# Performance work log

Measured on AMD Instinct MI355X. Metric: run time of the kernel, lower is better.

The kernel has to match this reference:

```python
import jax, jax.numpy as jnp
import numpy as np

B, L, D, N = 2, 2048, 1024, 16
DT_MIN, DT_MAX = 1e-3, 1e-1


def setup_inputs() -> dict:
    key = jax.random.key(0)
    ks = jax.random.split(key, 8)
    u = jax.random.normal(ks[0], (B, L, D), dtype=jnp.float32)
    # torch.nn.Linear weights are (out_features, in_features)
    W_dt = jax.random.normal(ks[1], (D, D), dtype=jnp.float32) * 0.02
    b_dt = jnp.zeros((D,), dtype=jnp.float32)
    W_B = jax.random.normal(ks[2], (D * N, D), dtype=jnp.float32) * 0.02
    b_B = jnp.zeros((D * N,), dtype=jnp.float32)
    W_C = jax.random.normal(ks[3], (D * N, D), dtype=jnp.float32) * 0.02
    b_C = jnp.zeros((D * N,), dtype=jnp.float32)
    # log_A init: log(1..N) broadcast over channels (HiPPO-ish diagonal)
    log_A = jnp.broadcast_to(jnp.log(jnp.arange(1, N + 1, dtype=jnp.float32)), (D, N))
    D_skip = jnp.ones((D,), dtype=jnp.float32)
    lo, hi = float(np.log(DT_MIN)), float(np.log(DT_MAX))
    dt_bias = jax.random.uniform(ks[4], (D,), dtype=jnp.float32) * (hi - lo) + lo
    return {"u": u, "log_A": log_A, "D_skip": D_skip, "dt_bias": dt_bias,
            "W_dt": W_dt, "b_dt": b_dt, "W_B": W_B, "b_B": b_B,
            "W_C": W_C, "b_C": b_C}


def reference(u, log_A, D_skip, dt_bias, W_dt, b_dt, W_B, b_B, W_C, b_C):
    b, l, d = u.shape
    n = log_A.shape[1]
    A = -jnp.exp(log_A)                                   # (d, n), A < 0
    # token-dependent parameters, computed for all timesteps at once
    dt = jax.nn.softplus(u @ W_dt.T + b_dt + dt_bias)     # (b, l, d)
    Bt = (u @ W_B.T + b_B).reshape(b, l, d, n)            # (b, l, d, n)
    Ct = (u @ W_C.T + b_C).reshape(b, l, d, n)            # (b, l, d, n)
    # exact ZOH discretisation
    A_bar = jnp.exp(dt[..., None] * A)                    # (b, l, d, n)
    B_bar = (A_bar - 1.0) / A * Bt                        # (b, l, d, n)
    x_in = B_bar * u[..., None]                           # (b, l, d, n)
    # recurrent scan over time
    def step(h, inp):
        a_t, x_t, c_t = inp                               # each (b, d, n)
        h = a_t * h + x_t
        y_t = jnp.sum(c_t * h, axis=-1)                   # (b, d)
        return h, y_t
    h0 = jnp.zeros((b, d, n), dtype=u.dtype)
    xs = (jnp.moveaxis(A_bar, 1, 0), jnp.moveaxis(x_in, 1, 0), jnp.moveaxis(Ct, 1, 0))
    _, ys = jax.lax.scan(step, h0, xs)                    # ys: (l, b, d)
    y = jnp.moveaxis(ys, 0, 1) + D_skip * u               # (b, l, d)
    return y
```

## Files before the change

### kernel.cpp

```cpp
#include <hip/hip_runtime.h>
#include <hip/hip_bf16.h>
#include <stdint.h>

constexpr int Bb = 2;
constexpr int Ll = 2048;
constexpr int Dd = 1024;
constexpr int Nn = 16;
constexpr int NB = Dd * Nn;
constexpr int SL = 64;
constexpr int NCH = Bb * Dd;
constexpr int KCAT = 3 * Dd;

typedef __bf16 bf16_t;
typedef __bf16 bf16x8 __attribute__((ext_vector_type(8)));
typedef __bf16 bf16x4 __attribute__((ext_vector_type(4)));
typedef float f32x4 __attribute__((ext_vector_type(4)));

__device__ inline void gld_lds16(const void* g, void* l) {
    __builtin_amdgcn_global_load_lds(
        (const __attribute__((address_space(1))) unsigned int*)g,
        (__attribute__((address_space(3))) unsigned int*)l, 16, 0, 0);
}

__global__ __launch_bounds__(256) void cvt_bf16(const float* __restrict__ s,
                                                bf16_t* __restrict__ d, int n4) {
    int i = blockIdx.x * 256 + threadIdx.x;
    const int stride = gridDim.x * 256;
    const float4* s4 = (const float4*)s;
    bf16x4* d4 = (bf16x4*)d;
    for (; i < n4; i += stride) {
        float4 v = s4[i];
        bf16x4 o = {(bf16_t)v.x, (bf16_t)v.y, (bf16_t)v.z, (bf16_t)v.w};
        d4[i] = o;
    }
}

__global__ __launch_bounds__(256) void build_ucat(const float* __restrict__ u,
                                                  bf16_t* __restrict__ ucat) {
    const int i = blockIdx.x * 256 + threadIdx.x;
    const int row = i >> 8;
    const int c = (i & 255) << 2;
    float4 v = ((const float4*)u)[i];
    bf16x4 hi = {(bf16_t)v.x, (bf16_t)v.y, (bf16_t)v.z, (bf16_t)v.w};
    bf16x4 lo = {(bf16_t)(v.x - (float)hi.x), (bf16_t)(v.y - (float)hi.y),
                 (bf16_t)(v.z - (float)hi.z), (bf16_t)(v.w - (float)hi.w)};
    bf16_t* r = ucat + (size_t)row * KCAT;
    *(bf16x4*)(r + c) = hi;
    *(bf16x4*)(r + Dd + c) = lo;
    *(bf16x4*)(r + 2 * Dd + c) = hi;
}

__global__ __launch_bounds__(256) void build_wcat(const float* __restrict__ w,
                                                  bf16_t* __restrict__ wcat) {
    const int i = blockIdx.x * 256 + threadIdx.x;
    const int row = i >> 8;
    const int c = (i & 255) << 2;
    float4 v = ((const float4*)w)[i];
    bf16x4 hi = {(bf16_t)v.x, (bf16_t)v.y, (bf16_t)v.z, (bf16_t)v.w};
    bf16x4 lo = {(bf16_t)(v.x - (float)hi.x), (bf16_t)(v.y - (float)hi.y),
                 (bf16_t)(v.z - (float)hi.z), (bf16_t)(v.w - (float)hi.w)};
    bf16_t* r = wcat + (size_t)row * KCAT;
    *(bf16x4*)(r + c) = hi;
    *(bf16x4*)(r + Dd + c) = hi;
    *(bf16x4*)(r + 2 * Dd + c) = lo;
}

template <int EP, typename OutT>
__global__ __launch_bounds__(256) void gemm_mfma(
    const bf16_t* __restrict__ Abase, int CL, int l0, int K,
    const bf16_t* __restrict__ W, const float* __restrict__ b1,
    const float* __restrict__ b2, OutT* __restrict__ C, int N)
{
    __shared__ bf16_t As[128 * 32];
    __shared__ bf16_t Bs[128 * 32];

    const int tid = threadIdx.x;
    const int bn = blockIdx.x * 128;
    const int rglob = blockIdx.y * 128;
    const int batch = rglob / CL;
    const int rin = rglob % CL;
    const bf16_t* Ap = Abase + ((size_t)batch * Ll + l0 + rin) * K;
    const bf16_t* Wp = W + (size_t)bn * K;
    OutT* Cp = C + (size_t)rglob * N;

    const int sr = tid >> 2;
    const int sc = (tid & 3) << 3;
    char* ldsA = (char*)As + tid * 16;
    char* ldsB = (char*)Bs + tid * 16;

    const int lane = tid & 63;
    const int wid = tid >> 6;
    const int wm = (wid & 1) << 6;
    const int wn = (wid >> 1) << 6;
    const int lr = lane & 15;
    const int lq = lane >> 4;

    f32x4 acc[4][4] = {};

    for (int k0 = 0; k0 < K; k0 += 32) {
        __syncthreads();
        gld_lds16(Ap + (size_t)sr * K + k0 + sc, ldsA);
        gld_lds16(Ap + (size_t)(sr + 64) * K + k0 + sc, ldsA + 4096);
        gld_lds16(Wp + (size_t)sr * K + k0 + sc, ldsB);
        gld_lds16(Wp + (size_t)(sr + 64) * K + k0 + sc, ldsB + 4096);
        __syncthreads();

        bf16x8 af[4], bfr[4];
#pragma unroll
        for (int mi = 0; mi < 4; ++mi)
            af[mi] = *(const bf16x8*)&As[(wm + mi * 16 + lr) * 32 + lq * 8];
#pragma unroll
        for (int ni = 0; ni < 4; ++ni)
            bfr[ni] = *(const bf16x8*)&Bs[(wn + ni * 16 + lr) * 32 + lq * 8];
#pragma unroll
        for (int mi = 0; mi < 4; ++mi)
#pragma unroll
            for (int ni = 0; ni < 4; ++ni)
                acc[mi][ni] = __builtin_amdgcn_mfma_f32_16x16x32_bf16(
                    af[mi], bfr[ni], acc[mi][ni], 0, 0, 0);
    }

#pragma unroll
    for (int ni = 0; ni < 4; ++ni) {
        const int col = bn + wn + ni * 16 + lr;
        const float bc = b1[col] + (EP == 1 ? b2[col] : 0.f);
#pragma unroll
        for (int mi = 0; mi < 4; ++mi)
#pragma unroll
            for (int i = 0; i < 4; ++i) {
                float v = acc[mi][ni][i] + bc;
                if (EP == 1) v = (v > 20.f) ? v : log1pf(__expf(v));
                Cp[(size_t)(wm + mi * 16 + lq * 4 + i) * N + col] = (OutT)v;
            }
    }
}

__global__ __launch_bounds__(512, 2) void gemm256(
    const bf16_t* __restrict__ Abase, int CL, int l0, int K,
    const bf16_t* __restrict__ W, const float* __restrict__ b1,
    bf16_t* __restrict__ C, int N)
{
    extern __shared__ char smem[];
    const int tid = threadIdx.x;
    const int bn = blockIdx.x * 256;
    const int rglob = blockIdx.y * 256;
    const int batch = rglob / CL;
    const int rin = rglob % CL;
    const bf16_t* Ap = Abase + ((size_t)batch * Ll + l0 + rin) * K;
    const bf16_t* Wp = W + (size_t)bn * K;
    bf16_t* Cp = C + (size_t)rglob * N;

    const int lane = tid & 63;
    const int wid = tid >> 6;
    const int wr = wid >> 2;
    const int wc = wid & 3;
    const int lr = lane & 15;
    const int lq = lane >> 4;
    const int NT = K >> 6;

    const int c0 = tid, c1 = tid + 512;
    const int r0 = c0 >> 3, r1 = c1 >> 3;
    const int kb0 = ((c0 & 7) << 3) ^ ((r0 & 7) << 3);
    const int kb1 = ((c1 & 7) << 3) ^ ((r1 & 7) << 3);

    auto stage = [&](const bf16_t* src, char* dst, int tt, int h) {
        gld_lds16(src + (size_t)(h * 128 + r0) * K + tt * 64 + kb0,
                  dst + h * 16384 + c0 * 16);
        gld_lds16(src + (size_t)(h * 128 + r1) * K + tt * 64 + kb1,
                  dst + h * 16384 + c1 * 16);
    };

    stage(Ap, smem, 0, 0);
    stage(Ap, smem, 0, 1);
    stage(Wp, smem + 32768, 0, 0);
    stage(Wp, smem + 32768, 0, 1);
    if (NT > 1) {
        stage(Wp, smem + 65536 + 32768, 1, 0);
        stage(Wp, smem + 65536 + 32768, 1, 1);
        asm volatile("s_waitcnt vmcnt(4)" ::: "memory");
    } else {
        asm volatile("s_waitcnt vmcnt(0)" ::: "memory");
    }
    __builtin_amdgcn_s_barrier();

    f32x4 acc[8][4] = {};
    const int xsw = (lr & 7) << 4;

    for (int t = 0; t < NT; ++t) {
        char* Ard = smem + ((t & 1) ? 65536 : 0);
        char* Brd = Ard + 32768;
        char* Awr = smem + ((t & 1) ? 0 : 65536);
        char* Bwr = Brd;

        bf16x8 bfr[2][4];
#pragma unroll
        for (int p = 0; p < 4; ++p) {
            if (p == 0) { if (t + 1 < NT) stage(Ap, Awr, t + 1, 0); }
            if (p == 1) { if (t + 1 < NT) stage(Ap, Awr, t + 1, 1); }
            if (p == 2) { if (t + 2 < NT) stage(Wp, Bwr, t + 2, 0); }
            if (p == 3) { if (t + 2 < NT) stage(Wp, Bwr, t + 2, 1); }

            if (p == 0) {
#pragma unroll
                for (int ks = 0; ks < 2; ++ks)
#pragma unroll
                    for (int ni = 0; ni < 4; ++ni)
                        bfr[ks][ni] = *(const bf16x8*)(Brd +
                            (wc * 64 + ni * 16 + lr) * 128 +
                            ((ks * 64 + lq * 16) ^ xsw));
            }
            bf16x8 a0k0 = *(const bf16x8*)(Ard +
                (wr * 128 + (2 * p) * 16 + lr) * 128 + ((lq * 16) ^ xsw));
            bf16x8 a0k1 = *(const bf16x8*)(Ard +
                (wr * 128 + (2 * p) * 16 + lr) * 128 + ((64 + lq * 16) ^ xsw));
            bf16x8 a1k0 = *(const bf16x8*)(Ard +
                (wr * 128 + (2 * p + 1) * 16 + lr) * 128 + ((lq * 16) ^ xsw));
            bf16x8 a1k1 = *(const bf16x8*)(Ard +
                (wr * 128 + (2 * p + 1) * 16 + lr) * 128 + ((64 + lq * 16) ^ xsw));

            __builtin_amdgcn_s_barrier();
            __builtin_amdgcn_s_setprio(1);
#pragma unroll
            for (int ni = 0; ni < 4; ++ni) {
                acc[2 * p][ni] = __builtin_amdgcn_mfma_f32_16x16x32_bf16(
                    a0k0, bfr[0][ni], acc[2 * p][ni], 0, 0, 0);
                acc[2 * p][ni] = __builtin_amdgcn_mfma_f32_16x16x32_bf16(
                    a0k1, bfr[1][ni], acc[2 * p][ni], 0, 0, 0);
                acc[2 * p + 1][ni] = __builtin_amdgcn_mfma_f32_16x16x32_bf16(
                    a1k0, bfr[0][ni], acc[2 * p + 1][ni], 0, 0, 0);
                acc[2 * p + 1][ni] = __builtin_amdgcn_mfma_f32_16x16x32_bf16(
                    a1k1, bfr[1][ni], acc[2 * p + 1][ni], 0, 0, 0);
            }
            __builtin_amdgcn_s_setprio(0);
            if (p == 3) {
                if (t + 2 < NT)
                    asm volatile("s_waitcnt vmcnt(4)" ::: "memory");
                else if (t + 1 < NT)
                    asm volatile("s_waitcnt vmcnt(0)" ::: "memory");
            }
            __builtin_amdgcn_s_barrier();
        }
    }

#pragma unroll
    for (int ni = 0; ni < 4; ++ni) {
        const int col = bn + wc * 64 + ni * 16 + lr;
        const float bc = b1[col];
#pragma unroll
        for (int mi = 0; mi < 8; ++mi)
#pragma unroll
            for (int i = 0; i < 4; ++i)
                Cp[(size_t)(wr * 128 + mi * 16 + lq * 4 + i) * N + col] =
                    (bf16_t)(acc[mi][ni][i] + bc);
    }
}

__global__ __launch_bounds__(256) void scan_seg_local(
    const float* __restrict__ u, const float* __restrict__ dt,
    const bf16_t* __restrict__ Bt_c, const float* __restrict__ log_A,
    float* __restrict__ pseg, float* __restrict__ hseg, int CL, int l0)
{
    const int tid = threadIdx.x;
    const int g = tid >> 4, n = tid & 15;
    const int gid = blockIdx.x * 16 + g;
    const int ch = gid & (NCH - 1);
    const int s = gid >> 11;
    const int b = ch >> 10, d = ch & (Dd - 1);

    const float A = -__expf(log_A[d * Nn + n]);
    const float rA = 1.f / A;

    size_t idx_bn = (size_t)(b * CL + s * SL) * NB + d * Nn + n;
    size_t idx_u = ((size_t)b * Ll + l0 + s * SL) * Dd + d;

    float p = 1.f, h = 0.f;
    for (int l = 0; l < SL; ++l) {
        const float dtv = dt[idx_u];
        const float uv = u[idx_u];
        const float bv = (float)Bt_c[idx_bn];
        const float a = __expf(dtv * A);
        p *= a;
        h = a * h + (a - 1.f) * rA * bv * uv;
        idx_bn += NB; idx_u += Dd;
    }
    const size_t o = ((size_t)s * NCH + ch) * Nn + n;
    pseg[o] = p;
    hseg[o] = h;
}

__global__ __launch_bounds__(256) void scan_combine(
    const float* __restrict__ pseg, const float* __restrict__ hseg,
    float* __restrict__ hin_arr, float* __restrict__ h_state,
    int NSEG, int l0)
{
    const int t = blockIdx.x * 256 + threadIdx.x;
    float hin = (l0 == 0) ? 0.f : h_state[t];
    for (int s = 0; s < NSEG; ++s) {
        const size_t o = (size_t)s * (NCH * Nn) + t;
        hin_arr[o] = hin;
        hin = pseg[o] * hin + hseg[o];
    }
    h_state[t] = hin;
}

__global__ __launch_bounds__(256) void scan_seg_final(
    const float* __restrict__ u, const float* __restrict__ dt,
    const bf16_t* __restrict__ Bt_c, const bf16_t* __restrict__ Ct_c,
    const float* __restrict__ log_A, const float* __restrict__ D_skip,
    const float* __restrict__ hin_arr, float* __restrict__ y, int CL, int l0)
{
    const int tid = threadIdx.x;
    const int g = tid >> 4, n = tid & 15;
    const int gid = blockIdx.x * 16 + g;
    const int ch = gid & (NCH - 1);
    const int s = gid >> 11;
    const int b = ch >> 10, d = ch & (Dd - 1);

    const float A = -__expf(log_A[d * Nn + n]);
    const float rA = 1.f / A;
    const float Dsk = D_skip[d];

    size_t idx_bn = (size_t)(b * CL + s * SL) * NB + d * Nn + n;
    size_t idx_u = ((size_t)b * Ll + l0 + s * SL) * Dd + d;

    float h = hin_arr[((size_t)s * NCH + ch) * Nn + n];
    for (int l = 0; l < SL; ++l) {
        const float dtv = dt[idx_u];
        const float uv = u[idx_u];
        const float bv = (float)Bt_c[idx_bn];
        const float cv = (float)Ct_c[idx_bn];
        const float a = __expf(dtv * A);
        h = a * h + (a - 1.f) * rA * bv * uv;
        float p = cv * h;
        p += __shfl_xor(p, 1);
        p += __shfl_xor(p, 2);
        p += __shfl_xor(p, 4);
        p += __shfl_xor(p, 8);
        if (n == 0) y[idx_u] = p + Dsk * uv;
        idx_bn += NB; idx_u += Dd;
    }
}

static inline size_t al256(size_t x) { return (x + 255) & ~(size_t)255; }

extern "C" void kernel_launch(void* const* d_in, const int* in_sizes, int n_in,
                              void* d_out, int out_size, void* d_ws, size_t ws_size,
                              hipStream_t stream) {
    const float* u       = (const float*)d_in[0];
    const float* log_A   = (const float*)d_in[1];
    const float* D_skip  = (const float*)d_in[2];
    const float* dt_bias = (const float*)d_in[3];
    const float* W_dt    = (const float*)d_in[4];
    const float* b_dt    = (const float*)d_in[5];
    const float* W_B     = (const float*)d_in[6];
    const float* b_B     = (const float*)d_in[7];
    const float* W_C     = (const float*)d_in[8];
    const float* b_C     = (const float*)d_in[9];
    float* y = (float*)d_out;

    hipFuncSetAttribute(reinterpret_cast<const void*>(gemm256),
                        hipFuncAttributeMaxDynamicSharedMemorySize, 131072);

    const size_t sz_ubf  = al256((size_t)Bb * Ll * Dd * 2);
    const size_t sz_w    = al256((size_t)NB * Dd * 2);
    const size_t sz_h    = al256((size_t)NCH * Nn * 4);
    const size_t sz_dtf  = al256((size_t)Bb * Ll * Dd * 4);
    const size_t sz_ucat = al256((size_t)Bb * Ll * KCAT * 2);
    const size_t sz_wcat = al256((size_t)Dd * KCAT * 2);

    int CL = 128;
    const int cands[5] = {2048, 1024, 512, 256, 128};
    for (int i = 0; i < 5; ++i) {
        const int c = cands[i];
        const int nseg = c / SL;
        const size_t seg = 3 * al256((size_t)nseg * NCH * Nn * 4);
        const size_t chunk = 2 * al256((size_t)2 * c * NB * 2);
        const size_t ovl = sz_ucat + sz_wcat;
        const size_t need = sz_ubf + 2 * sz_w + sz_h + sz_dtf + seg +
                            (chunk > ovl ? chunk : ovl);
        if (need <= ws_size) { CL = c; break; }
    }
    const int NSEG = CL / SL;

    char* p = (char*)d_ws;
    bf16_t* u_bf   = (bf16_t*)p; p += sz_ubf;
    bf16_t* wB_bf  = (bf16_t*)p; p += sz_w;
    bf16_t* wC_bf  = (bf16_t*)p; p += sz_w;
    float* h_state = (float*)p; p += sz_h;
    float* dt_full = (float*)p; p += sz_dtf;
    const size_t sz_seg1 = al256((size_t)NSEG * NCH * Nn * 4);
    float* pseg    = (float*)p; p += sz_seg1;
    float* hseg    = (float*)p; p += sz_seg1;
    float* hin_arr = (float*)p; p += sz_seg1;
    char* chunk0 = p;
    bf16_t* Bt_c = (bf16_t*)chunk0;
    bf16_t* Ct_c = (bf16_t*)(chunk0 + al256((size_t)2 * CL * NB * 2));
    bf16_t* u_cat = (bf16_t*)chunk0;
    bf16_t* w_cat = (bf16_t*)(chunk0 + sz_ucat);

    cvt_bf16<<<2048, 256, 0, stream>>>(u, u_bf, Bb * Ll * Dd / 4);
    cvt_bf16<<<2048, 256, 0, stream>>>(W_B, wB_bf, NB * Dd / 4);
    cvt_bf16<<<2048, 256, 0, stream>>>(W_C, wC_bf, NB * Dd / 4);
    build_ucat<<<Bb * Ll * Dd / 4 / 256, 256, 0, stream>>>(u, u_cat);
    build_wcat<<<Dd * Dd / 4 / 256, 256, 0, stream>>>(W_dt, w_cat);

    gemm_mfma<1, float><<<dim3(Dd / 128, Bb * Ll / 128), 256, 0, stream>>>(
        u_cat, Ll, 0, KCAT, w_cat, b_dt, dt_bias, dt_full, Dd);

    const bool use256 = (CL % 256 == 0);
    for (int l0 = 0; l0 < Ll; l0 += CL) {
        if (use256) {
            gemm256<<<dim3(NB / 256, 2 * CL / 256), 512, 131072, stream>>>(
                u_bf, CL, l0, Dd, wB_bf, b_B, Bt_c, NB);
            gemm256<<<dim3(NB / 256, 2 * CL / 256), 512, 131072, stream>>>(
                u_bf, CL, l0, Dd, wC_bf, b_C, Ct_c, NB);
        } else {
            gemm_mfma<0, bf16_t><<<dim3(NB / 128, 2 * CL / 128), 256, 0, stream>>>(
                u_bf, CL, l0, Dd, wB_bf, b_B, nullptr, Bt_c, NB);
            gemm_mfma<0, bf16_t><<<dim3(NB / 128, 2 * CL / 128), 256, 0, stream>>>(
                u_bf, CL, l0, Dd, wC_bf, b_C, nullptr, Ct_c, NB);
        }
        scan_seg_local<<<dim3(128 * NSEG), 256, 0, stream>>>(
            u, dt_full, Bt_c, log_A, pseg, hseg, CL, l0);
        scan_combine<<<dim3(128), 256, 0, stream>>>(
            pseg, hseg, hin_arr, h_state, NSEG, l0);
        scan_seg_final<<<dim3(128 * NSEG), 256, 0, stream>>>(
            u, dt_full, Bt_c, Ct_c, log_A, D_skip, hin_arr, y, CL, l0);
    }
}
```

Baseline: 730.5 us.

## Merge B and C projection GEMMs into one launch with swizzled tile order

Replaces the two per-chunk gemm256 launches for the B and C projections with a single gemm256_bc kernel. Each block picks the B or C weight from its flattened block id, using a grouped tile ordering meant to improve L2 reuse of the shared u tiles. The MFMA operands are swapped so each lane holds four consecutive output columns, which lets the epilogue write vectorized bf16x4 stores with float4 bias loads. A separate smaller-tile gemm_dt kernel computes dt with vectorized float4 softplus stores. The cost is more kernel code and a dt kernel with single-buffered LDS staging.

```diff
diff --git a/kernel.cpp b/kernel.cpp
--- a/kernel.cpp
+++ b/kernel.cpp
@@ -135,20 +135,103 @@
     }
 }
 
-__global__ __launch_bounds__(512, 2) void gemm256(
+__global__ __launch_bounds__(256) void gemm_dt(
+    const bf16_t* __restrict__ A, int K, const bf16_t* __restrict__ W,
+    const float* __restrict__ b1, const float* __restrict__ b2,
+    float* __restrict__ C)
+{
+    __shared__ bf16_t As[128 * 32];
+    __shared__ bf16_t Bs[64 * 32];
+
+    const int tid = threadIdx.x;
+    const int bn = blockIdx.x * 64;
+    const int row0 = blockIdx.y * 128;
+    const bf16_t* Ap = A + (size_t)row0 * K;
+    const bf16_t* Wp = W + (size_t)bn * K;
+    float* Cp = C + (size_t)row0 * Dd;
+
+    const int sr = tid >> 2;
+    const int sc = (tid & 3) << 3;
+    char* ldsA = (char*)As + tid * 16;
+    char* ldsB = (char*)Bs + tid * 16;
+
+    const int lane = tid & 63;
+    const int wid = tid >> 6;
+    const int wm = (wid & 1) << 6;
+    const int wn = (wid >> 1) << 5;
+    const int lr = lane & 15;
+    const int lq = lane >> 4;
+
+    f32x4 acc[4][2] = {};
+
+    for (int k0 = 0; k0 < K; k0 += 32) {
+        __syncthreads();
+        gld_lds16(Ap + (size_t)sr * K + k0 + sc, ldsA);
+        gld_lds16(Ap + (size_t)(sr + 64) * K + k0 + sc, ldsA + 4096);
+        gld_lds16(Wp + (size_t)sr * K + k0 + sc, ldsB);
+        __syncthreads();
+
+        bf16x8 af[4], bfr[2];
+#pragma unroll
+        for (int mi = 0; mi < 4; ++mi)
+            af[mi] = *(const bf16x8*)&As[(wm + mi * 16 + lr) * 32 + lq * 8];
+#pragma unroll
+        for (int ni = 0; ni < 2; ++ni)
+            bfr[ni] = *(const bf16x8*)&Bs[(wn + ni * 16 + lr) * 32 + lq * 8];
+#pragma unroll
+        for (int mi = 0; mi < 4; ++mi)
+#pragma unroll
+            for (int ni = 0; ni < 2; ++ni)
+                acc[mi][ni] = __builtin_amdgcn_mfma_f32_16x16x32_bf16(
+                    bfr[ni], af[mi], acc[mi][ni], 0, 0, 0);
+    }
+
+#pragma unroll
+    for (int ni = 0; ni < 2; ++ni) {
+        const int col = bn + wn + ni * 16 + lq * 4;
+        const float4 ba = *(const float4*)&b1[col];
+        const float4 bb = *(const float4*)&b2[col];
+        const float bc[4] = {ba.x + bb.x, ba.y + bb.y, ba.z + bb.z, ba.w + bb.w};
+#pragma unroll
+        for (int mi = 0; mi < 4; ++mi) {
+            const int row = wm + mi * 16 + lr;
+            f32x4 v;
+#pragma unroll
+            for (int i = 0; i < 4; ++i) {
+                float t = acc[mi][ni][i] + bc[i];
+                v[i] = (t > 20.f) ? t : log1pf(__expf(t));
+            }
+            *(f32x4*)(Cp + (size_t)row * Dd + col) = v;
+        }
+    }
+}
+
+__global__ __launch_bounds__(512, 2) void gemm256_bc(
     const bf16_t* __restrict__ Abase, int CL, int l0, int K,
-    const bf16_t* __restrict__ W, const float* __restrict__ b1,
-    bf16_t* __restrict__ C, int N)
+    const bf16_t* __restrict__ WB, const bf16_t* __restrict__ WC,
+    const float* __restrict__ bB, const float* __restrict__ bC,
+    bf16_t* __restrict__ OB, bf16_t* __restrict__ OC)
 {
     extern __shared__ char smem[];
     const int tid = threadIdx.x;
-    const int bn = blockIdx.x * 256;
-    const int rglob = blockIdx.y * 256;
+
+    const int NY = (2 * CL) >> 8;
+    const int id = blockIdx.x;
+    const int cx = id & 7;
+    const int jj = id >> 3;
+    const int x = cx * 16 + jj / NY;
+    const int yb = jj % NY;
+
+    const int rglob = yb * 256;
     const int batch = rglob / CL;
     const int rin = rglob % CL;
     const bf16_t* Ap = Abase + ((size_t)batch * Ll + l0 + rin) * K;
-    const bf16_t* Wp = W + (size_t)bn * K;
-    bf16_t* Cp = C + (size_t)rglob * N;
+
+    const bf16_t* Wp; const float* bias; bf16_t* Co; int bn;
+    if (x < 64) { Wp = WB; bias = bB; Co = OB; bn = x * 256; }
+    else        { Wp = WC; bias = bC; Co = OC; bn = (x - 64) * 256; }
+    Wp += (size_t)bn * K;
+    bf16_t* Cp = Co + (size_t)rglob * NB;
 
     const int lane = tid & 63;
     const int wid = tid >> 6;
@@ -223,13 +306,13 @@
 #pragma unroll
             for (int ni = 0; ni < 4; ++ni) {
                 acc[2 * p][ni] = __builtin_amdgcn_mfma_f32_16x16x32_bf16(
-                    a0k0, bfr[0][ni], acc[2 * p][ni], 0, 0, 0);
+                    bfr[0][ni], a0k0, acc[2 * p][ni], 0, 0, 0);
                 acc[2 * p][ni] = __builtin_amdgcn_mfma_f32_16x16x32_bf16(
-                    a0k1, bfr[1][ni], acc[2 * p][ni], 0, 0, 0);
+                    bfr[1][ni], a0k1, acc[2 * p][ni], 0, 0, 0);
                 acc[2 * p + 1][ni] = __builtin_amdgcn_mfma_f32_16x16x32_bf16(
-                    a1k0, bfr[0][ni], acc[2 * p + 1][ni], 0, 0, 0);
+                    bfr[0][ni], a1k0, acc[2 * p + 1][ni], 0, 0, 0);
                 acc[2 * p + 1][ni] = __builtin_amdgcn_mfma_f32_16x16x32_bf16(
-                    a1k1, bfr[1][ni], acc[2 * p + 1][ni], 0, 0, 0);
+                    bfr[1][ni], a1k1, acc[2 * p + 1][ni], 0, 0, 0);
             }
             __builtin_amdgcn_s_setprio(0);
             if (p == 3) {
@@ -242,16 +325,22 @@
         }
     }
 
-#pragma unroll
-    for (int ni = 0; ni < 4; ++ni) {
-        const int col = bn + wc * 64 + ni * 16 + lr;
-        const float bc = b1[col];
-#pragma unroll
-        for (int mi = 0; mi < 8; ++mi)
-#pragma unroll
-            for (int i = 0; i < 4; ++i)
-                Cp[(size_t)(wr * 128 + mi * 16 + lq * 4 + i) * N + col] =
-                    (bf16_t)(acc[mi][ni][i] + bc);
+    float4 bv[4];
+#pragma unroll
+    for (int ni = 0; ni < 4; ++ni)
+        bv[ni] = *(const float4*)&bias[bn + wc * 64 + ni * 16 + lq * 4];
+#pragma unroll
+    for (int mi = 0; mi < 8; ++mi) {
+        const size_t rowoff = (size_t)(wr * 128 + mi * 16 + lr) * NB;
+#pragma unroll
+        for (int ni = 0; ni < 4; ++ni) {
+            const int col = bn + wc * 64 + ni * 16 + lq * 4;
+            bf16x4 o = {(bf16_t)(acc[mi][ni][0] + bv[ni].x),
+                        (bf16_t)(acc[mi][ni][1] + bv[ni].y),
+                        (bf16_t)(acc[mi][ni][2] + bv[ni].z),
+                        (bf16_t)(acc[mi][ni][3] + bv[ni].w)};
+            *(bf16x4*)(Cp + rowoff + col) = o;
+        }
     }
 }
 
@@ -358,7 +447,7 @@
     const float* b_C     = (const float*)d_in[9];
     float* y = (float*)d_out;
 
-    hipFuncSetAttribute(reinterpret_cast<const void*>(gemm256),
+    hipFuncSetAttribute(reinterpret_cast<const void*>(gemm256_bc),
                         hipFuncAttributeMaxDynamicSharedMemorySize, 131072);
 
     const size_t sz_ubf  = al256((size_t)Bb * Ll * Dd * 2);
@@ -404,16 +493,15 @@
     build_ucat<<<Bb * Ll * Dd / 4 / 256, 256, 0, stream>>>(u, u_cat);
     build_wcat<<<Dd * Dd / 4 / 256, 256, 0, stream>>>(W_dt, w_cat);
 
-    gemm_mfma<1, float><<<dim3(Dd / 128, Bb * Ll / 128), 256, 0, stream>>>(
-        u_cat, Ll, 0, KCAT, w_cat, b_dt, dt_bias, dt_full, Dd);
+    gemm_dt<<<dim3(Dd / 64, Bb * Ll / 128), 256, 0, stream>>>(
+        u_cat, KCAT, w_cat, b_dt, dt_bias, dt_full);
 
     const bool use256 = (CL % 256 == 0);
     for (int l0 = 0; l0 < Ll; l0 += CL) {
         if (use256) {
-            gemm256<<<dim3(NB / 256, 2 * CL / 256), 512, 131072, stream>>>(
-                u_bf, CL, l0, Dd, wB_bf, b_B, Bt_c, NB);
-            gemm256<<<dim3(NB / 256, 2 * CL / 256), 512, 131072, stream>>>(
-                u_bf, CL, l0, Dd, wC_bf, b_C, Ct_c, NB);
+            const int NY = 2 * CL / 256;
+            gemm256_bc<<<dim3(128 * NY), 512, 131072, stream>>>(
+                u_bf, CL, l0, Dd, wB_bf, wC_bf, b_B, b_C, Bt_c, Ct_c);
         } else {
             gemm_mfma<0, bf16_t><<<dim3(NB / 128, 2 * CL / 128), 256, 0, stream>>>(
                 u_bf, CL, l0, Dd, wB_bf, b_B, nullptr, Bt_c, NB);
```

Result: faster. 689.1 us (-5.7%).
